# Performance work log

Measured on AMD Instinct MI355X. Metric: run time of the kernel, lower is better.

The kernel has to match this reference:

```python
import jax, jax.numpy as jnp
import numpy as np

EMBED = 768
HEADS = 12
HEAD_DIM = EMBED // HEADS  # 64


def setup_inputs() -> dict:
    key = jax.random.key(0)
    ks = jax.random.split(key, 9)
    d = HEAD_DIM
    s = 1.0 / np.sqrt(d)
    return {
        "x": jax.random.normal(ks[0], (8, 1024, EMBED), dtype=jnp.float32),
        "ln_w": jnp.ones((EMBED,), dtype=jnp.float32),
        "ln_b": jnp.zeros((EMBED,), dtype=jnp.float32),
        "Wq": jax.random.uniform(ks[1], (d, d), jnp.float32, -s, s),
        "bq": jax.random.uniform(ks[2], (d,), jnp.float32, -s, s),
        "Wk": jax.random.uniform(ks[3], (d, d), jnp.float32, -s, s),
        "bk": jax.random.uniform(ks[4], (d,), jnp.float32, -s, s),
        "Wv": jax.random.uniform(ks[5], (d, d), jnp.float32, -s, s),
        "bv": jax.random.uniform(ks[6], (d,), jnp.float32, -s, s),
    }


def reference(x, ln_w, ln_b, Wq, bq, Wk, bk, Wv, bv):
    bs, n, e = x.shape
    # LayerNorm over last dim (eps matches torch default 1e-5)
    mu = jnp.mean(x, axis=-1, keepdims=True)
    var = jnp.mean(jnp.square(x - mu), axis=-1, keepdims=True)
    xn = (x - mu) / jnp.sqrt(var + 1e-5) * ln_w + ln_b
    # Raw view split (NOT transpose split): [bs, n, E] -> [bs, H, n, d]
    xh = xn.reshape(bs, HEADS, n, HEAD_DIM)
    # Linear layers (torch Linear: y = x @ W.T + b)
    q = jnp.einsum("bhnd,ed->bhne", xh, Wq) + bq
    k = jnp.einsum("bhnd,ed->bhne", xh, Wk) + bk
    v = jnp.einsum("bhnd,ed->bhne", xh, Wv) + bv
    # Unusual: softmax FIRST, then divide by sqrt(d)
    scores = jnp.einsum("bhqd,bhkd->bhqk", q, k)
    attn = jax.nn.softmax(scores, axis=-1) / jnp.sqrt(jnp.float32(HEAD_DIM))
    feature = jnp.einsum("bhqk,bhkd->bhqd", attn, v)
    return feature.reshape(bs, n, e)
```

## Files before the change

kernel.cpp:

```cpp
#include <hip/hip_runtime.h>

#define EMBED 768
#define HEADS 12
#define HD 64
#define SEQ 1024
#define BS 8
#define NROWS (BS * HEADS * SEQ)
#define XP 72
#define PLP 40

typedef _Float16 f16;
typedef f16 f16x4 __attribute__((ext_vector_type(4)));
typedef f16 f16x8 __attribute__((ext_vector_type(8)));
typedef float f32x4 __attribute__((ext_vector_type(4)));

__global__ __launch_bounds__(256) void k_lnstats(const float* __restrict__ x,
                                                 const float* __restrict__ Wq,
                                                 const float* __restrict__ Wk,
                                                 const float* __restrict__ Wv,
                                                 float* __restrict__ mu_out,
                                                 float* __restrict__ rs_out,
                                                 f16* __restrict__ wf) {
    const int w = threadIdx.x >> 6;
    const int lane = threadIdx.x & 63;
    const int row = blockIdx.x * 4 + w;
    const float4* xr = (const float4*)(x + (long)row * EMBED);
    float s = 0.f, sq = 0.f;
#pragma unroll
    for (int kk = 0; kk < 3; ++kk) {
        float4 v = xr[lane + kk * 64];
        s += v.x + v.y + v.z + v.w;
        sq += v.x * v.x + v.y * v.y + v.z * v.z + v.w * v.w;
    }
#pragma unroll
    for (int off = 32; off; off >>= 1) {
        s += __shfl_xor(s, off, 64);
        sq += __shfl_xor(sq, off, 64);
    }
    if (lane == 0) {
        float mu = s * (1.f / EMBED);
        float var = sq * (1.f / EMBED) - mu * mu;
        mu_out[row] = mu;
        rs_out[row] = rsqrtf(var + 1e-5f);
    }
    if (blockIdx.x < 3) {
        const float* W = (blockIdx.x == 0) ? Wq : (blockIdx.x == 1) ? Wk : Wv;
        f16* dst = wf + (long)blockIdx.x * 4096;
        const int t = threadIdx.x;
#pragma unroll
        for (int i = 0; i < 2; ++i) {
            const int o = t * 2 + i;
            const int nt = o >> 7, half = (o >> 6) & 1, lp = o & 63;
            const int qd = lp >> 4, l16 = lp & 15;
            const float* src = W + (nt * 16 + l16) * 64 + half * 32 + qd * 8;
            float4 v0 = *(const float4*)src, v1 = *(const float4*)(src + 4);
            f16x8 h = {(f16)v0.x, (f16)v0.y, (f16)v0.z, (f16)v0.w,
                       (f16)v1.x, (f16)v1.y, (f16)v1.z, (f16)v1.w};
            *(f16x8*)(dst + o * 8) = h;
        }
    }
}

__global__ __launch_bounds__(256) void k_qkv(
    const float* __restrict__ x, const float* __restrict__ lw, const float* __restrict__ lb,
    const f16* __restrict__ wf,
    const float* __restrict__ bq, const float* __restrict__ bk, const float* __restrict__ bv,
    const float* __restrict__ mu, const float* __restrict__ rs,
    f16* __restrict__ qo, f16* __restrict__ ko, f16* __restrict__ vo) {
    __shared__ __align__(16) f16 xh[2][64 * XP];
    const int t = threadIdx.x;
    const unsigned r0 = (unsigned)blockIdx.x * 128;
    const int bh = (int)(r0 >> 10);
    const int seq0 = (int)(r0 & 1023);
    const int tile0 = seq0 >> 5;

#pragma unroll
    for (int st = 0; st < 2; ++st) {
        const unsigned fb = (r0 + st * 64u) * 64u + (unsigned)t * 16u;
        const unsigned xrow = fb / EMBED;
        const unsigned c0 = fb % EMBED;
        const float m_ = mu[xrow], s_ = rs[xrow];
        const int lrow = (t * 16) >> 6, lcol = (t * 16) & 63;
        f16* dst = &xh[st][lrow * XP + lcol];
        const float4* xp = (const float4*)(x + fb);
        const float4* wp = (const float4*)(lw + c0);
        const float4* bp = (const float4*)(lb + c0);
#pragma unroll
        for (int j = 0; j < 4; ++j) {
            float4 xv = xp[j], wv = wp[j], bv2 = bp[j];
            f16x4 h = {(f16)((xv.x - m_) * s_ * wv.x + bv2.x), (f16)((xv.y - m_) * s_ * wv.y + bv2.y),
                       (f16)((xv.z - m_) * s_ * wv.z + bv2.z), (f16)((xv.w - m_) * s_ * wv.w + bv2.w)};
            *(f16x4*)(dst + j * 4) = h;
        }
    }
    __syncthreads();

    const int lane = t & 63, w = t >> 6, l16 = lane & 15, quad = lane >> 4;
    f16x8 a[2][2];
#pragma unroll
    for (int st = 0; st < 2; ++st) {
        a[st][0] = *(const f16x8*)&xh[st][(w * 16 + l16) * XP + quad * 8];
        a[st][1] = *(const f16x8*)&xh[st][(w * 16 + l16) * XP + 32 + quad * 8];
    }
    const float* Bs[3] = {bq, bk, bv};

#pragma unroll
    for (int m = 0; m < 3; ++m) {
        const f16* wfm = wf + (long)m * 4096 + lane * 8;
        f32x4 acc[2][4];
#pragma unroll
        for (int nt = 0; nt < 4; ++nt) {
            f16x8 b0 = *(const f16x8*)(wfm + (nt * 2 + 0) * 512);
            f16x8 b1 = *(const f16x8*)(wfm + (nt * 2 + 1) * 512);
            const float bias = Bs[m][nt * 16 + l16];
#pragma unroll
            for (int st = 0; st < 2; ++st) {
                f32x4 a_ = {0.f, 0.f, 0.f, 0.f};
                a_ = __builtin_amdgcn_mfma_f32_16x16x32_f16(a[st][0], b0, a_, 0, 0, 0);
                a_ = __builtin_amdgcn_mfma_f32_16x16x32_f16(a[st][1], b1, a_, 0, 0, 0);
#pragma unroll
                for (int rg = 0; rg < 4; ++rg) a_[rg] += bias;
                acc[st][nt] = a_;
            }
        }

        __syncthreads();
        if (m < 2) {
#pragma unroll
            for (int st = 0; st < 2; ++st)
#pragma unroll
                for (int nt = 0; nt < 4; ++nt)
#pragma unroll
                    for (int rg = 0; rg < 4; ++rg)
                        xh[st][(w * 16 + quad * 4 + rg) * XP + nt * 16 + l16] = (f16)acc[st][nt][rg];
        } else {
#pragma unroll
            for (int st = 0; st < 2; ++st)
#pragma unroll
                for (int nt = 0; nt < 4; ++nt) {
                    f16x4 h = {(f16)acc[st][nt][0], (f16)acc[st][nt][1], (f16)acc[st][nt][2], (f16)acc[st][nt][3]};
                    *(f16x4*)&xh[st][(nt * 16 + l16) * XP + w * 16 + quad * 4] = h;
                }
        }
        __syncthreads();
        if (m == 0) {
#pragma unroll
            for (int st = 0; st < 2; ++st)
#pragma unroll
                for (int c = t; c < 512; c += 256) {
                    const int row = c >> 3, c8 = (c & 7) * 8;
                    *(f16x8*)(qo + ((long)r0 + st * 64 + row) * 64 + c8) = *(const f16x8*)&xh[st][row * XP + c8];
                }
        } else if (m == 1) {
#pragma unroll
            for (int st = 0; st < 2; ++st) {
                f16* kb = ko + ((long)bh << 16) + (long)(tile0 + st * 2) * 2048;
#pragma unroll
                for (int c = t; c < 512; c += 256) {
                    const int tl = c >> 8, chunk = (c >> 6) & 3, qd = (c >> 4) & 3, l16s = c & 15;
                    const int row = tl * 32 + (chunk >> 1) * 16 + l16s;
                    const int col = (chunk & 1) * 32 + qd * 8;
                    *(f16x8*)(kb + (long)c * 8) = *(const f16x8*)&xh[st][row * XP + col];
                }
            }
        } else {
#pragma unroll
            for (int st = 0; st < 2; ++st) {
                f16* vb = vo + ((long)bh << 16) + (long)(tile0 + st * 2) * 2048;
#pragma unroll
                for (int c = t; c < 512; c += 256) {
                    const int tl = c >> 8, nt = (c >> 6) & 3, qd = (c >> 4) & 3, l16d = c & 15;
                    const f16* base = &xh[st][(nt * 16 + l16d) * XP + tl * 32 + qd * 4];
                    f16x4 lo = *(const f16x4*)base;
                    f16x4 hi = *(const f16x4*)(base + 16);
                    f16x8 o8 = {lo[0], hi[0], lo[1], hi[1], lo[2], hi[2], lo[3], hi[3]};
                    *(f16x8*)(vb + (long)c * 8) = o8;
                }
            }
        }
    }
}

__global__ __launch_bounds__(256) void k_attn(const f16* __restrict__ q,
                                              const f16* __restrict__ k,
                                              const f16* __restrict__ vt,
                                              float* __restrict__ out) {
    __shared__ __align__(16) f16 pl[4][32 * PLP];
    const int t = threadIdx.x;
    const int w = t >> 6, lane = t & 63, l16 = lane & 15, quad = lane >> 4;
    const int bh = blockIdx.x;
    const int q0 = blockIdx.y * 128 + w * 32;
    const long hb = (long)bh * SEQ;
    const f16* kp0 = k + ((long)bh << 16) + lane * 8;
    const f16* vp0 = vt + ((long)bh << 16) + lane * 8;

    f16x8 qf[2][2];
#pragma unroll
    for (int mt = 0; mt < 2; ++mt) {
        const f16* qp = q + (hb + q0 + mt * 16 + l16) * 64 + quad * 8;
        qf[mt][0] = *(const f16x8*)qp;
        qf[mt][1] = *(const f16x8*)(qp + 32);
    }
    f32x4 o[2][4];
    f32x4 ls[2];
#pragma unroll
    for (int mt = 0; mt < 2; ++mt) {
        ls[mt] = (f32x4){0.f, 0.f, 0.f, 0.f};
#pragma unroll
        for (int nt = 0; nt < 4; ++nt) o[mt][nt] = (f32x4){0.f, 0.f, 0.f, 0.f};
    }
    f16x8 one;
#pragma unroll
    for (int j = 0; j < 8; ++j) one[j] = (f16)1.0f;
    const f32x4 m14 = {-14.f, -14.f, -14.f, -14.f};

#define LOADK(kt, kf)                                  \
    {                                                  \
        const f16* kp = kp0 + (kt) * 2048;             \
        kf[0] = *(const f16x8*)kp;                     \
        kf[1] = *(const f16x8*)(kp + 512);             \
        kf[2] = *(const f16x8*)(kp + 1024);            \
        kf[3] = *(const f16x8*)(kp + 1536);            \
    }
#define LOADV(kt, vf)                                  \
    {                                                  \
        const f16* vp = vp0 + (kt) * 2048;             \
        vf[0] = *(const f16x8*)vp;                     \
        vf[1] = *(const f16x8*)(vp + 512);             \
        vf[2] = *(const f16x8*)(vp + 1024);            \
        vf[3] = *(const f16x8*)(vp + 1536);            \
    }

    f16x8 ka[4], va[4], kb[4], vb[4];
    LOADK(0, ka);
    LOADV(0, va);

    auto body = [&](const f16x8* kf, const f16x8* vf) {
        f32x4 s[2][2];
#pragma unroll
        for (int mt = 0; mt < 2; ++mt) {
            f32x4 a = m14;
            a = __builtin_amdgcn_mfma_f32_16x16x32_f16(qf[mt][0], kf[0], a, 0, 0, 0);
            a = __builtin_amdgcn_mfma_f32_16x16x32_f16(qf[mt][1], kf[1], a, 0, 0, 0);
            s[mt][0] = a;
            f32x4 b = m14;
            b = __builtin_amdgcn_mfma_f32_16x16x32_f16(qf[mt][0], kf[2], b, 0, 0, 0);
            b = __builtin_amdgcn_mfma_f32_16x16x32_f16(qf[mt][1], kf[3], b, 0, 0, 0);
            s[mt][1] = b;
        }
#pragma unroll
        for (int mt = 0; mt < 2; ++mt)
#pragma unroll
            for (int rg = 0; rg < 4; ++rg) {
                float e0 = __expf(s[mt][0][rg]);
                float e1 = __expf(s[mt][1][rg]);
                auto pk = __builtin_amdgcn_cvt_pkrtz(e0, e1);
                *(decltype(pk)*)&pl[w][(mt * 16 + quad * 4 + rg) * PLP + l16 * 2] = pk;
            }
        f16x8 pf0 = *(const f16x8*)&pl[w][l16 * PLP + quad * 8];
        f16x8 pf1 = *(const f16x8*)&pl[w][(16 + l16) * PLP + quad * 8];
        ls[0] = __builtin_amdgcn_mfma_f32_16x16x32_f16(pf0, one, ls[0], 0, 0, 0);
        ls[1] = __builtin_amdgcn_mfma_f32_16x16x32_f16(pf1, one, ls[1], 0, 0, 0);
#pragma unroll
        for (int nt = 0; nt < 4; ++nt) {
            o[0][nt] = __builtin_amdgcn_mfma_f32_16x16x32_f16(pf0, vf[nt], o[0][nt], 0, 0, 0);
            o[1][nt] = __builtin_amdgcn_mfma_f32_16x16x32_f16(pf1, vf[nt], o[1][nt], 0, 0, 0);
        }
    };

    for (int kt = 0; kt < SEQ / 32; kt += 2) {
        LOADK(kt + 1, kb);
        LOADV(kt + 1, vb);
        body(ka, va);
        const int kn = (kt + 2 < SEQ / 32) ? kt + 2 : SEQ / 32 - 1;
        LOADK(kn, ka);
        LOADV(kn, va);
        body(kb, vb);
    }
#undef LOADK
#undef LOADV

#pragma unroll
    for (int mt = 0; mt < 2; ++mt) {
        float inv[4];
#pragma unroll
        for (int rg = 0; rg < 4; ++rg) inv[rg] = 1.f / (ls[mt][rg] * 8.0f);
#pragma unroll
        for (int nt = 0; nt < 4; ++nt) {
            float* op = out + (hb + q0 + mt * 16 + quad * 4) * 64 + nt * 16 + l16;
#pragma unroll
            for (int rg = 0; rg < 4; ++rg) op[(long)rg * 64] = o[mt][nt][rg] * inv[rg];
        }
    }
}

extern "C" void kernel_launch(void* const* d_in, const int* in_sizes, int n_in,
                              void* d_out, int out_size, void* d_ws, size_t ws_size,
                              hipStream_t stream) {
    const float* x = (const float*)d_in[0];
    const float* lw = (const float*)d_in[1];
    const float* lb = (const float*)d_in[2];
    const float* Wq = (const float*)d_in[3];
    const float* bq = (const float*)d_in[4];
    const float* Wk = (const float*)d_in[5];
    const float* bk = (const float*)d_in[6];
    const float* Wv = (const float*)d_in[7];
    const float* bv = (const float*)d_in[8];
    float* out = (float*)d_out;

    char* ws = (char*)d_ws;
    float* mu = (float*)ws;
    float* rs = (float*)(ws + 32768);
    f16* wfr = (f16*)(ws + 65536);
    f16* qo = (f16*)(ws + 98304);
    f16* ko = qo + (long)NROWS * 64;
    f16* vo = ko + (long)NROWS * 64;

    k_lnstats<<<2048, 256, 0, stream>>>(x, Wq, Wk, Wv, mu, rs, wfr);
    k_qkv<<<NROWS / 128, 256, 0, stream>>>(x, lw, lb, wfr, bq, bk, bv, mu, rs, qo, ko, vo);
    k_attn<<<dim3(BS * HEADS, SEQ / 128), 256, 0, stream>>>(qo, ko, vo, out);
}
```

Measured before the change: 139.6 us.

## Stage K and V tiles in dedicated shared buffers and cut QKV barriers

The QKV projection kernel now writes K and V straight into new shared-memory buffers already laid out in the global tile order. All global stores for Q, K and V happen once, after a single barrier at the end. The per-projection barriers and the barrier after the LayerNorm staging are removed, which relies on each wave reading only the xh rows it wrote itself. This trades roughly 32KB of extra shared memory per block, with possible occupancy loss, for fewer block-wide barriers and fewer shared-memory round trips.

```diff
diff --git a/kernel.cpp b/kernel.cpp
--- a/kernel.cpp
+++ b/kernel.cpp
@@ -68,6 +68,8 @@
     const float* __restrict__ mu, const float* __restrict__ rs,
     f16* __restrict__ qo, f16* __restrict__ ko, f16* __restrict__ vo) {
     __shared__ __align__(16) f16 xh[2][64 * XP];
+    __shared__ __align__(16) f16 kb[2][4096];
+    __shared__ __align__(16) f16 vb[2][4096];
     const int t = threadIdx.x;
     const unsigned r0 = (unsigned)blockIdx.x * 128;
     const int bh = (int)(r0 >> 10);
@@ -93,7 +95,6 @@
             *(f16x4*)(dst + j * 4) = h;
         }
     }
-    __syncthreads();
 
     const int lane = t & 63, w = t >> 6, l16 = lane & 15, quad = lane >> 4;
     f16x8 a[2][2];
@@ -123,9 +124,7 @@
                 acc[st][nt] = a_;
             }
         }
-
-        __syncthreads();
-        if (m < 2) {
+        if (m == 0) {
 #pragma unroll
             for (int st = 0; st < 2; ++st)
 #pragma unroll
@@ -133,50 +132,49 @@
 #pragma unroll
                     for (int rg = 0; rg < 4; ++rg)
                         xh[st][(w * 16 + quad * 4 + rg) * XP + nt * 16 + l16] = (f16)acc[st][nt][rg];
+        } else if (m == 1) {
+#pragma unroll
+            for (int st = 0; st < 2; ++st)
+#pragma unroll
+                for (int nt = 0; nt < 4; ++nt) {
+                    const int base = (w >> 1) * 2048 + ((w & 1) * 2 + (nt >> 1)) * 512 +
+                                     ((((nt & 1) << 1) | (l16 >> 3))) * 128 + (quad * 4) * 8 + (l16 & 7);
+#pragma unroll
+                    for (int rg = 0; rg < 4; ++rg)
+                        kb[st][base + rg * 8] = (f16)acc[st][nt][rg];
+                }
         } else {
 #pragma unroll
             for (int st = 0; st < 2; ++st)
 #pragma unroll
                 for (int nt = 0; nt < 4; ++nt) {
-                    f16x4 h = {(f16)acc[st][nt][0], (f16)acc[st][nt][1], (f16)acc[st][nt][2], (f16)acc[st][nt][3]};
-                    *(f16x4*)&xh[st][(nt * 16 + l16) * XP + w * 16 + quad * 4] = h;
+                    const int base = (w >> 1) * 2048 + nt * 512 + quad * 128 + l16 * 8 + (w & 1);
+#pragma unroll
+                    for (int rg = 0; rg < 4; ++rg)
+                        vb[st][base + rg * 2] = (f16)acc[st][nt][rg];
                 }
         }
-        __syncthreads();
-        if (m == 0) {
-#pragma unroll
-            for (int st = 0; st < 2; ++st)
-#pragma unroll
-                for (int c = t; c < 512; c += 256) {
-                    const int row = c >> 3, c8 = (c & 7) * 8;
-                    *(f16x8*)(qo + ((long)r0 + st * 64 + row) * 64 + c8) = *(const f16x8*)&xh[st][row * XP + c8];
-                }
-        } else if (m == 1) {
-#pragma unroll
-            for (int st = 0; st < 2; ++st) {
-                f16* kb = ko + ((long)bh << 16) + (long)(tile0 + st * 2) * 2048;
-#pragma unroll
-                for (int c = t; c < 512; c += 256) {
-                    const int tl = c >> 8, chunk = (c >> 6) & 3, qd = (c >> 4) & 3, l16s = c & 15;
-                    const int row = tl * 32 + (chunk >> 1) * 16 + l16s;
-                    const int col = (chunk & 1) * 32 + qd * 8;
-                    *(f16x8*)(kb + (long)c * 8) = *(const f16x8*)&xh[st][row * XP + col];
-                }
-            }
-        } else {
-#pragma unroll
-            for (int st = 0; st < 2; ++st) {
-                f16* vb = vo + ((long)bh << 16) + (long)(tile0 + st * 2) * 2048;
-#pragma unroll
-                for (int c = t; c < 512; c += 256) {
-                    const int tl = c >> 8, nt = (c >> 6) & 3, qd = (c >> 4) & 3, l16d = c & 15;
-                    const f16* base = &xh[st][(nt * 16 + l16d) * XP + tl * 32 + qd * 4];
-                    f16x4 lo = *(const f16x4*)base;
-                    f16x4 hi = *(const f16x4*)(base + 16);
-                    f16x8 o8 = {lo[0], hi[0], lo[1], hi[1], lo[2], hi[2], lo[3], hi[3]};
-                    *(f16x8*)(vb + (long)c * 8) = o8;
-                }
-            }
+    }
+
+    __syncthreads();
+
+#pragma unroll
+    for (int st = 0; st < 2; ++st)
+#pragma unroll
+        for (int c = t; c < 512; c += 256) {
+            const int row = c >> 3, c8 = (c & 7) * 8;
+            *(f16x8*)(qo + ((long)r0 + st * 64 + row) * 64 + c8) = *(const f16x8*)&xh[st][row * XP + c8];
+        }
+    {
+        f16* kg = ko + ((long)bh << 16) + (long)tile0 * 2048;
+        f16* vg = vo + ((long)bh << 16) + (long)tile0 * 2048;
+        const f16* kfl = &kb[0][0];
+        const f16* vfl = &vb[0][0];
+#pragma unroll
+        for (int i = 0; i < 4; ++i) {
+            const int o = (t + i * 256) * 8;
+            *(f16x8*)(kg + o) = *(const f16x8*)(kfl + o);
+            *(f16x8*)(vg + o) = *(const f16x8*)(vfl + o);
         }
     }
 }
```

After: 138.8 us. Within noise of the previous version (-0.6%).
